# Optimization experiments

Hardware: AMD Instinct MI355X
Metric: run time of the kernel (lower is better)

The kernel has to match this reference:

```python
import jax, jax.numpy as jnp
import numpy as np

N_PATHS = 1_000_000
N_LINKS = 50_000
K_HOPS = 8


def setup_inputs() -> dict:
    key = jax.random.key(0)
    k1, k2, k3 = jax.random.split(key, 3)
    # path features; column 1 is the injected traffic A (as in X[:, path_og.stop-2])
    P = jax.random.uniform(k1, (N_PATHS, 3), dtype=jnp.float32)
    # raw link capacity feature data.L; forward divides by 1000 -> capacity in [100, 300]
    L = jax.random.uniform(k2, (N_LINKS, 1), dtype=jnp.float32) * 2.0e5 + 1.0e5
    # k-th hop of each path: which path (global node id == local id since paths come first)
    pl_paths = jnp.broadcast_to(jnp.arange(N_PATHS, dtype=jnp.int32), (K_HOPS, N_PATHS))
    # which link node id is traversed at hop k (global ids: links occupy [N_PATHS, N_PATHS+N_LINKS))
    pl_edges = jax.random.randint(k3, (K_HOPS, N_PATHS), N_PATHS, N_PATHS + N_LINKS, dtype=jnp.int32)
    return {"P": P, "L": L, "pl_paths": pl_paths, "pl_edges": pl_edges,
            "n_paths": N_PATHS, "n_links": N_LINKS, "num_iterations": 3}


def reference(P, L, pl_paths, pl_edges, n_paths, n_links, num_iterations):
    B = 32  # buffer size
    A = P[:, 1]                      # per-path injected traffic [n_paths]
    cap = L[:, 0] / 1000.0           # link capacity (X[is_l, link_og.start]) [n_links]
    e_local = pl_edges - n_paths     # link-local indices [K, n_paths]

    def update_traffic(bp_links):
        # Original: at step k, decay traffic by prev step's blocking then scatter.
        # Equivalent reorder: scatter this step, then decay with this step's links
        # (decayed traffic is only consumed at step k+1).
        def step(carry, xs):
            traffic, T = carry
            pk, ek = xs
            T = T + jax.ops.segment_sum(traffic[pk], ek, num_segments=n_links)
            traffic = traffic.at[pk].multiply(1.0 - bp_links[ek])
            return (traffic, T), None
        T0 = jnp.zeros((n_links,), dtype=A.dtype)
        (_, T), _ = jax.lax.scan(step, (A, T0), (pl_paths, e_local))
        return T

    bp = 0.5 * jnp.ones((n_links,), dtype=A.dtype)
    rho = jnp.zeros((n_links,), dtype=A.dtype)
    for _ in range(num_iterations):
        T = update_traffic(bp)
        rho = T / cap
        bp = (1.0 - rho) * rho ** B / (1.0 - rho ** (B + 1) + 1e-8)

    # Erlang-like mean-queue series: res = pi0 * (1 + sum_{m=1}^{32} m*rho^m) / 32
    pi0 = (1.0 - rho) / (1.0 - rho ** (B + 1))
    m = jnp.arange(B + 1, dtype=A.dtype)            # [33]
    coeff = jnp.where(m == 0, 1.0, m)
    Lq = pi0 * jnp.sum(coeff * rho[:, None] ** m, axis=1) / 32.0   # [n_links]
    pi0_final = pi0 * rho ** B                       # pi_0 after the 32-step loop

    # final per-path delay aggregation over all path-link edges
    X_l = Lq * 32000.0 / L[:, 0]                     # [n_links]
    E = X_l[e_local.reshape(-1)]                     # [K*n_paths]
    res = jax.ops.segment_sum(E, pl_paths.reshape(-1), num_segments=n_paths)
    return res, jnp.stack([Lq, rho, pi0_final], axis=1)
```

## Files before the change

kernel.cpp:

```cpp
#include <hip/hip_runtime.h>

#define KHOPS  8
#define BS     1024
#define MAXL   50176
#define HWORDS (MAXL / 2)
#define GRID   256
#define NXCD   8
#define RPQ    (GRID / NXCD)
#define TSCALE  2048.0f
#define XSCALE  131072.0f

typedef unsigned char  u8;
typedef unsigned short u16;
typedef unsigned int   u32;

__device__ __forceinline__ void deposit(u32* h, u32 link, float t) {
    atomicAdd(&h[link >> 1], __float2uint_rn(t * TSCALE) << ((link & 1) << 4));
}

__global__ __launch_bounds__(BS) void scatter_first(
        const float* __restrict__ P,
        const int*   __restrict__ pl_edges,
        u16*   __restrict__ e16,
        float* __restrict__ A,
        u32*   __restrict__ Trep,
        int n_paths, int nwords) {
    __shared__ u32 h[HWORDS];
    const int tid = threadIdx.x;
    const int nthreads = gridDim.x * BS;

    for (int i = tid; i < HWORDS; i += BS) h[i] = 0u;
    __syncthreads();

    for (int p = (blockIdx.x * BS + tid) * 4; p < n_paths; p += 4 * nthreads) {
        uint2 ep[KHOPS];
#pragma unroll
        for (int k = 0; k < KHOPS; ++k) {
            int4 e4 = *(const int4*)&pl_edges[k * n_paths + p];
            ep[k].x = (u32)(e4.x - n_paths) | ((u32)(e4.y - n_paths) << 16);
            ep[k].y = (u32)(e4.z - n_paths) | ((u32)(e4.w - n_paths) << 16);
            *(uint2*)&e16[k * n_paths + p] = ep[k];
        }
        float4 q0 = *(const float4*)&P[3 * p];
        float4 q1 = *(const float4*)&P[3 * p + 4];
        float4 q2 = *(const float4*)&P[3 * p + 8];
        float t0 = q0.y, t1 = q1.x, t2 = q1.w, t3 = q2.z;
        *(float4*)&A[p] = make_float4(t0, t1, t2, t3);
#pragma unroll
        for (int k = 0; k < KHOPS; ++k) {
            deposit(h, ep[k].x & 0xffffu, t0);
            deposit(h, ep[k].x >> 16,     t1);
            deposit(h, ep[k].y & 0xffffu, t2);
            deposit(h, ep[k].y >> 16,     t3);
            t0 *= 0.5f; t1 *= 0.5f; t2 *= 0.5f; t3 *= 0.5f;
        }
    }
    __syncthreads();

    u32* Tmine = Trep + (size_t)blockIdx.x * nwords;
    for (int i = tid; i < nwords; i += BS) Tmine[i] = h[i];
}

__global__ __launch_bounds__(BS) void scatter_rest(
        const float* __restrict__ A,
        const u16*   __restrict__ e16,
        const u8*    __restrict__ bpq,
        u32*         __restrict__ Trep,
        int n_paths, int n_links, int nwords) {
    __shared__ u8  bpl[MAXL];
    __shared__ u32 h[HWORDS];
    const int tid = threadIdx.x;
    const int nthreads = gridDim.x * BS;

    for (int i = tid; i < n_links; i += BS) bpl[i] = bpq[i];
    for (int i = tid; i < HWORDS; i += BS) h[i] = 0u;
    __syncthreads();

    for (int p = (blockIdx.x * BS + tid) * 4; p < n_paths; p += 4 * nthreads) {
        uint2 ep[KHOPS];
#pragma unroll
        for (int k = 0; k < KHOPS; ++k)
            ep[k] = *(const uint2*)&e16[k * n_paths + p];
        float4 a = *(const float4*)&A[p];
        float t0 = a.x, t1 = a.y, t2 = a.z, t3 = a.w;
#pragma unroll
        for (int k = 0; k < KHOPS; ++k) {
            u32 l0 = ep[k].x & 0xffffu, l1 = ep[k].x >> 16;
            u32 l2 = ep[k].y & 0xffffu, l3 = ep[k].y >> 16;
            deposit(h, l0, t0);
            deposit(h, l1, t1);
            deposit(h, l2, t2);
            deposit(h, l3, t3);
            t0 *= (float)(256 - (int)bpl[l0]) * (1.0f / 256.0f);
            t1 *= (float)(256 - (int)bpl[l1]) * (1.0f / 256.0f);
            t2 *= (float)(256 - (int)bpl[l2]) * (1.0f / 256.0f);
            t3 *= (float)(256 - (int)bpl[l3]) * (1.0f / 256.0f);
        }
    }
    __syncthreads();

    u32* Tmine = Trep + (size_t)blockIdx.x * nwords;
    for (int i = tid; i < nwords; i += BS) Tmine[i] = h[i];
}

__global__ __launch_bounds__(BS) void merge_kernel(
        const u32* __restrict__ Trep,
        u32* __restrict__ partial,
        int n_links, int nwords) {
    const int q = blockIdx.x & (NXCD - 1);
    const int w = (blockIdx.x >> 3) * BS + threadIdx.x;
    if (w >= nwords) return;
    u32 slo = 0, shi = 0;
#pragma unroll 4
    for (int j = 0; j < RPQ; ++j) {
        u32 v = Trep[(size_t)(q + NXCD * j) * nwords + w];
        slo += v & 0xffffu;
        shi += v >> 16;
    }
    *(uint2*)&partial[(size_t)q * n_links + 2 * w] = make_uint2(slo, shi);
}

__global__ void link_update_kernel(const float* __restrict__ L,
                                   const u32*   __restrict__ partial,
                                   u8*          __restrict__ bpq,
                                   u16*         __restrict__ xq,
                                   float*       __restrict__ out_links,
                                   int n_links, int last) {
    int l = blockIdx.x * blockDim.x + threadIdx.x;
    if (l >= n_links) return;
    u32 s = 0;
#pragma unroll
    for (int q = 0; q < NXCD; ++q)
        s += partial[(size_t)q * n_links + l];
    float T   = (float)s * (1.0f / TSCALE);
    float cap = L[l] * (1.0f / 1000.0f);
    float rho = T / cap;
    float r2 = rho * rho, r4 = r2 * r2, r8 = r4 * r4, r16 = r8 * r8;
    float r32 = r16 * r16, r33 = r32 * rho;
    if (!last) {
        float bp = (1.0f - rho) * r32 / (1.0f - r33 + 1e-8f);
        u32 b = __float2uint_rn(bp * 256.0f);
        bpq[l] = (u8)(b > 255u ? 255u : b);
    } else {
        float pi0 = (1.0f - rho) / (1.0f - r33);
        float S = 1.0f, rp = 1.0f;
#pragma unroll
        for (int m = 1; m <= 32; ++m) { rp *= rho; S += (float)m * rp; }
        float Lq = pi0 * S * (1.0f / 32.0f);
        float X  = Lq * 32000.0f / L[l];
        u32 xf = __float2uint_rn(X * XSCALE);
        xq[l] = (u16)(xf > 65535u ? 65535u : xf);
        out_links[3 * l + 0] = Lq;
        out_links[3 * l + 1] = rho;
        out_links[3 * l + 2] = pi0 * r32;
    }
}

__global__ __launch_bounds__(BS) void gather_kernel(
        const u16* __restrict__ e16,
        const u16* __restrict__ xq,
        float*     __restrict__ res,
        int n_paths, int n_links) {
    __shared__ u16 xl[MAXL];
    const int tid = threadIdx.x;
    for (int i = tid; i < n_links; i += BS) xl[i] = xq[i];
    __syncthreads();

    const int nthreads = gridDim.x * BS;
    for (int p = (blockIdx.x * BS + tid) * 4; p < n_paths; p += 4 * nthreads) {
        u32 s0 = 0, s1 = 0, s2 = 0, s3 = 0;
#pragma unroll
        for (int k = 0; k < KHOPS; ++k) {
            uint2 ep = *(const uint2*)&e16[k * n_paths + p];
            s0 += xl[ep.x & 0xffffu];
            s1 += xl[ep.x >> 16];
            s2 += xl[ep.y & 0xffffu];
            s3 += xl[ep.y >> 16];
        }
        *(float4*)&res[p] = make_float4((float)s0 * (1.0f / XSCALE),
                                        (float)s1 * (1.0f / XSCALE),
                                        (float)s2 * (1.0f / XSCALE),
                                        (float)s3 * (1.0f / XSCALE));
    }
}

extern "C" void kernel_launch(void* const* d_in, const int* in_sizes, int n_in,
                              void* d_out, int out_size, void* d_ws, size_t ws_size,
                              hipStream_t stream) {
    const float* P        = (const float*)d_in[0];
    const float* L        = (const float*)d_in[1];
    const int*   pl_edges = (const int*)d_in[3];

    const int n_paths = in_sizes[0] / 3;
    const int n_links = in_sizes[1];
    const int n_edges = KHOPS * n_paths;
    const int nwords  = (n_links + 1) / 2;

    char* w = (char*)d_ws;
    u16*   e16 = (u16*)w;                     w += (size_t)n_edges * 2;
    w = (char*)(((size_t)w + 15) & ~15ull);
    float* A   = (float*)w;                   w += (size_t)n_paths * 4;
    u8*    bpq = (u8*)w;                      w += (size_t)n_links;
    w = (char*)(((size_t)w + 15) & ~15ull);
    u16*   xq  = (u16*)w;                     w += (size_t)n_links * 2;
    w = (char*)(((size_t)w + 15) & ~15ull);
    u32* partial = (u32*)w;                   w += (size_t)NXCD * n_links * 4;
    u32* Trep    = (u32*)w;

    float* res       = (float*)d_out;
    float* out_links = res + n_paths;

    const int bs = 256;
    const int gl = (n_links + bs - 1) / bs;
    const int gm = NXCD * ((nwords + BS - 1) / BS);

    for (int it = 0; it < 3; ++it) {
        if (it == 0)
            scatter_first<<<GRID, BS, 0, stream>>>(P, pl_edges, e16, A, Trep,
                                                   n_paths, nwords);
        else
            scatter_rest<<<GRID, BS, 0, stream>>>(A, e16, bpq, Trep,
                                                  n_paths, n_links, nwords);
        merge_kernel<<<gm, BS, 0, stream>>>(Trep, partial, n_links, nwords);
        link_update_kernel<<<gl, bs, 0, stream>>>(L, partial, bpq, xq,
                                                  out_links, n_links,
                                                  it == 2 ? 1 : 0);
    }
    gather_kernel<<<GRID, BS, 0, stream>>>(e16, xq, res, n_paths, n_links);
}
```

Measured before the change: 174.1 us.

## Fuse link update into scatter and gather kernels, recomputing per block

```diff
diff --git a/kernel.cpp b/kernel.cpp
--- a/kernel.cpp
+++ b/kernel.cpp
@@ -64,7 +64,8 @@
 __global__ __launch_bounds__(BS) void scatter_rest(
         const float* __restrict__ A,
         const u16*   __restrict__ e16,
-        const u8*    __restrict__ bpq,
+        const float* __restrict__ Lcap,
+        const u32*   __restrict__ partial,
         u32*         __restrict__ Trep,
         int n_paths, int n_links, int nwords) {
     __shared__ u8  bpl[MAXL];
@@ -72,7 +73,20 @@
     const int tid = threadIdx.x;
     const int nthreads = gridDim.x * BS;
 
-    for (int i = tid; i < n_links; i += BS) bpl[i] = bpq[i];
+    for (int l = tid; l < n_links; l += BS) {
+        u32 s = 0;
+#pragma unroll
+        for (int q = 0; q < NXCD; ++q)
+            s += partial[(size_t)q * n_links + l];
+        float T   = (float)s * (1.0f / TSCALE);
+        float cap = Lcap[l] * (1.0f / 1000.0f);
+        float rho = T / cap;
+        float r2 = rho * rho, r4 = r2 * r2, r8 = r4 * r4, r16 = r8 * r8;
+        float r32 = r16 * r16, r33 = r32 * rho;
+        float bp = (1.0f - rho) * r32 / (1.0f - r33 + 1e-8f);
+        u32 b = __float2uint_rn(bp * 256.0f);
+        bpl[l] = (u8)(b > 255u ? 255u : b);
+    }
     for (int i = tid; i < HWORDS; i += BS) h[i] = 0u;
     __syncthreads();
 
@@ -120,50 +134,43 @@
     *(uint2*)&partial[(size_t)q * n_links + 2 * w] = make_uint2(slo, shi);
 }
 
-__global__ void link_update_kernel(const float* __restrict__ L,
-                                   const u32*   __restrict__ partial,
-                                   u8*          __restrict__ bpq,
-                                   u16*         __restrict__ xq,
-                                   float*       __restrict__ out_links,
-                                   int n_links, int last) {
-    int l = blockIdx.x * blockDim.x + threadIdx.x;
-    if (l >= n_links) return;
-    u32 s = 0;
-#pragma unroll
-    for (int q = 0; q < NXCD; ++q)
-        s += partial[(size_t)q * n_links + l];
-    float T   = (float)s * (1.0f / TSCALE);
-    float cap = L[l] * (1.0f / 1000.0f);
-    float rho = T / cap;
-    float r2 = rho * rho, r4 = r2 * r2, r8 = r4 * r4, r16 = r8 * r8;
-    float r32 = r16 * r16, r33 = r32 * rho;
-    if (!last) {
-        float bp = (1.0f - rho) * r32 / (1.0f - r33 + 1e-8f);
-        u32 b = __float2uint_rn(bp * 256.0f);
-        bpq[l] = (u8)(b > 255u ? 255u : b);
-    } else {
-        float pi0 = (1.0f - rho) / (1.0f - r33);
-        float S = 1.0f, rp = 1.0f;
-#pragma unroll
-        for (int m = 1; m <= 32; ++m) { rp *= rho; S += (float)m * rp; }
-        float Lq = pi0 * S * (1.0f / 32.0f);
-        float X  = Lq * 32000.0f / L[l];
-        u32 xf = __float2uint_rn(X * XSCALE);
-        xq[l] = (u16)(xf > 65535u ? 65535u : xf);
-        out_links[3 * l + 0] = Lq;
-        out_links[3 * l + 1] = rho;
-        out_links[3 * l + 2] = pi0 * r32;
-    }
-}
-
-__global__ __launch_bounds__(BS) void gather_kernel(
-        const u16* __restrict__ e16,
-        const u16* __restrict__ xq,
-        float*     __restrict__ res,
+__global__ __launch_bounds__(BS) void finale_kernel(
+        const float* __restrict__ Lcap,
+        const u32*   __restrict__ partial,
+        const u16*   __restrict__ e16,
+        float* __restrict__ res,
+        float* __restrict__ out_links,
         int n_paths, int n_links) {
     __shared__ u16 xl[MAXL];
     const int tid = threadIdx.x;
-    for (int i = tid; i < n_links; i += BS) xl[i] = xq[i];
+    const int per = (n_links + (int)gridDim.x - 1) / (int)gridDim.x;
+    const int lo  = blockIdx.x * per;
+    const int hi  = (lo + per < n_links) ? lo + per : n_links;
+
+    for (int l = tid; l < n_links; l += BS) {
+        u32 s = 0;
+#pragma unroll
+        for (int q = 0; q < NXCD; ++q)
+            s += partial[(size_t)q * n_links + l];
+        float T   = (float)s * (1.0f / TSCALE);
+        float cap = Lcap[l] * (1.0f / 1000.0f);
+        float rho = T / cap;
+        float r2 = rho * rho, r4 = r2 * r2, r8 = r4 * r4, r16 = r8 * r8;
+        float r32 = r16 * r16, r33 = r32 * rho;
+        float pi0 = (1.0f - rho) / (1.0f - r33);
+        float S = 1.0f, rp = 1.0f;
+#pragma unroll
+        for (int m = 1; m <= 32; ++m) { rp *= rho; S += (float)m * rp; }
+        float Lq = pi0 * S * (1.0f / 32.0f);
+        float X  = Lq * 32000.0f / Lcap[l];
+        u32 xf = __float2uint_rn(X * XSCALE);
+        xl[l] = (u16)(xf > 65535u ? 65535u : xf);
+        if (l >= lo && l < hi) {
+            out_links[3 * l + 0] = Lq;
+            out_links[3 * l + 1] = rho;
+            out_links[3 * l + 2] = pi0 * r32;
+        }
+    }
     __syncthreads();
 
     const int nthreads = gridDim.x * BS;
@@ -188,7 +195,7 @@
                               void* d_out, int out_size, void* d_ws, size_t ws_size,
                               hipStream_t stream) {
     const float* P        = (const float*)d_in[0];
-    const float* L        = (const float*)d_in[1];
+    const float* Lcap     = (const float*)d_in[1];
     const int*   pl_edges = (const int*)d_in[3];
 
     const int n_paths = in_sizes[0] / 3;
@@ -200,18 +207,12 @@
     u16*   e16 = (u16*)w;                     w += (size_t)n_edges * 2;
     w = (char*)(((size_t)w + 15) & ~15ull);
     float* A   = (float*)w;                   w += (size_t)n_paths * 4;
-    u8*    bpq = (u8*)w;                      w += (size_t)n_links;
-    w = (char*)(((size_t)w + 15) & ~15ull);
-    u16*   xq  = (u16*)w;                     w += (size_t)n_links * 2;
-    w = (char*)(((size_t)w + 15) & ~15ull);
     u32* partial = (u32*)w;                   w += (size_t)NXCD * n_links * 4;
     u32* Trep    = (u32*)w;
 
     float* res       = (float*)d_out;
     float* out_links = res + n_paths;
 
-    const int bs = 256;
-    const int gl = (n_links + bs - 1) / bs;
     const int gm = NXCD * ((nwords + BS - 1) / BS);
 
     for (int it = 0; it < 3; ++it) {
@@ -219,12 +220,10 @@
             scatter_first<<<GRID, BS, 0, stream>>>(P, pl_edges, e16, A, Trep,
                                                    n_paths, nwords);
         else
-            scatter_rest<<<GRID, BS, 0, stream>>>(A, e16, bpq, Trep,
+            scatter_rest<<<GRID, BS, 0, stream>>>(A, e16, Lcap, partial, Trep,
                                                   n_paths, n_links, nwords);
         merge_kernel<<<gm, BS, 0, stream>>>(Trep, partial, n_links, nwords);
-        link_update_kernel<<<gl, bs, 0, stream>>>(L, partial, bpq, xq,
-                                                  out_links, n_links,
-                                                  it == 2 ? 1 : 0);
-    }
-    gather_kernel<<<GRID, BS, 0, stream>>>(e16, xq, res, n_paths, n_links);
-}
+    }
+    finale_kernel<<<GRID, BS, 0, stream>>>(Lcap, partial, e16, res, out_links,
+                                           n_paths, n_links);
+}
```

Result: slower. 254.6 us (+46.3%).
